# Optimization experiments

Hardware: AMD Instinct MI355X
Metric: run time of the kernel (lower is better)

## Reference

```python
import jax, jax.numpy as jnp
import numpy as np

RES = 32
EPS = 0.0


def setup_inputs() -> dict:
    key = jax.random.key(0)
    k1, k2 = jax.random.split(key)
    B, C, N = 32, 64, 8192
    features = jax.random.normal(k1, (B, C, N), dtype=jnp.float32)
    coords = jax.random.normal(k2, (B, 3, N), dtype=jnp.float32)
    return {"features": features, "coords": coords}


def reference(features, coords):
    R = RES
    B, C, N = features.shape
    # center coords per batch (mean over points)
    norm_coords = coords - jnp.mean(coords, axis=2, keepdims=True)  # [B,3,N]
    # normalize=True branch: divide by 2*max point L2 norm
    max_norm = jnp.max(jnp.linalg.norm(norm_coords, axis=1, keepdims=True),
                       axis=2, keepdims=True)  # [B,1,1]
    norm_coords = norm_coords / (max_norm * 2.0 + EPS) + 0.5
    # scale to voxel grid and clip
    norm_coords = jnp.clip(norm_coords * R, 0.0, R - 1)  # [B,3,N]
    vox = jnp.round(norm_coords).astype(jnp.int32)  # [B,3,N]
    # flat voxel index per point, offset per batch -> global segment id
    flat = (vox[:, 0] * R + vox[:, 1]) * R + vox[:, 2]  # [B,N]
    idx = (flat + jnp.arange(B, dtype=jnp.int32)[:, None] * (R ** 3)).reshape(-1)  # [B*N]
    num_seg = B * R ** 3
    cnt = jax.ops.segment_sum(jnp.ones((B * N,), features.dtype), idx,
                              num_segments=num_seg)  # [B*R^3]
    feat_pn = features.transpose(0, 2, 1).reshape(B * N, C)  # [B*N,C]
    sums = jax.ops.segment_sum(feat_pn, idx, num_segments=num_seg)  # [B*R^3,C]
    avg = sums / jnp.maximum(cnt, 1.0)[:, None]
    voxelized = avg.reshape(B, R, R, R, C).transpose(0, 4, 1, 2, 3)  # [B,C,R,R,R]
    return voxelized, norm_coords
```

## Files before the change

kernel.cpp:

```cpp
#include <hip/hip_runtime.h>

constexpr int B = 32, C = 64, N = 8192, R = 32, R3 = R * R * R;
constexpr int HALF = R3 / 2;
constexpr int T = 1024;
constexpr int PPT = N / T;

typedef float f32x4 __attribute__((ext_vector_type(4)));
typedef unsigned int u32x4 __attribute__((ext_vector_type(4)));

constexpr size_t IDX_OFF = 0;
constexpr size_t PF_OFF  = (size_t)B * N * 2;

__device__ __forceinline__ void lds_barrier() {
  asm volatile("s_waitcnt lgkmcnt(0)" ::: "memory");
  __builtin_amdgcn_s_barrier();
  __builtin_amdgcn_sched_barrier(0);
}

__global__ __launch_bounds__(1024) void prep_kernel(
    const float* __restrict__ coords, float* __restrict__ ncout,
    unsigned short* __restrict__ idx, float* __restrict__ pf) {
  __shared__ __align__(16) unsigned char smem[R3 * 4];
  double* sm = (double*)smem;
  float* smf = (float*)smem;
  unsigned int* cnt = (unsigned int*)smem;

  const int b = blockIdx.x;
  const int t = threadIdx.x;
  const float* cb = coords + (size_t)b * 3 * N;

  double sx = 0.0, sy = 0.0, sz = 0.0;
  for (int n = t; n < N; n += T) {
    sx += (double)cb[n];
    sy += (double)cb[N + n];
    sz += (double)cb[2 * N + n];
  }
  float mean[3];
  double vals[3] = {sx, sy, sz};
  for (int d = 0; d < 3; ++d) {
    sm[t] = vals[d];
    __syncthreads();
    for (int s = 512; s > 0; s >>= 1) {
      if (t < s) sm[t] += sm[t + s];
      __syncthreads();
    }
    mean[d] = (float)(sm[0] / (double)N);
    __syncthreads();
  }

  float mx = 0.0f;
  for (int n = t; n < N; n += T) {
    float dx = __fsub_rn(cb[n], mean[0]);
    float dy = __fsub_rn(cb[N + n], mean[1]);
    float dz = __fsub_rn(cb[2 * N + n], mean[2]);
    float n2 = __fadd_rn(__fadd_rn(__fmul_rn(dx, dx), __fmul_rn(dy, dy)),
                         __fmul_rn(dz, dz));
    mx = fmaxf(mx, n2);
  }
  smf[t] = mx;
  __syncthreads();
  for (int s = 512; s > 0; s >>= 1) {
    if (t < s) smf[t] = fmaxf(smf[t], smf[t + s]);
    __syncthreads();
  }
  const float dn = __fmul_rn(__fsqrt_rn(smf[0]), 2.0f);
  __syncthreads();

  const int n0 = t * PPT;
  const f32x4 xa = *(const f32x4*)(cb + n0);
  const f32x4 xc = *(const f32x4*)(cb + n0 + 4);
  const f32x4 ya = *(const f32x4*)(cb + N + n0);
  const f32x4 yc = *(const f32x4*)(cb + N + n0 + 4);
  const f32x4 za = *(const f32x4*)(cb + 2 * N + n0);
  const f32x4 zc = *(const f32x4*)(cb + 2 * N + n0 + 4);

  {
    u32x4* cz = (u32x4*)cnt;
    const u32x4 z4 = {0u, 0u, 0u, 0u};
#pragma unroll
    for (int k = 0; k < R3 / 4; k += T) cz[k + t] = z4;
  }
  lds_barrier();

  int iv[PPT];
  f32x4 o0[2], o1[2], o2[2];
#pragma unroll
  for (int h = 0; h < 2; ++h) {
    const f32x4 xs = h ? xc : xa;
    const f32x4 ys = h ? yc : ya;
    const f32x4 zs = h ? zc : za;
#pragma unroll
    for (int j = 0; j < 4; ++j) {
      float t0 = __fmul_rn(__fadd_rn(__fdiv_rn(__fsub_rn(xs[j], mean[0]), dn), 0.5f), 32.0f);
      float t1 = __fmul_rn(__fadd_rn(__fdiv_rn(__fsub_rn(ys[j], mean[1]), dn), 0.5f), 32.0f);
      float t2 = __fmul_rn(__fadd_rn(__fdiv_rn(__fsub_rn(zs[j], mean[2]), dn), 0.5f), 32.0f);
      t0 = fminf(fmaxf(t0, 0.0f), 31.0f);
      t1 = fminf(fmaxf(t1, 0.0f), 31.0f);
      t2 = fminf(fmaxf(t2, 0.0f), 31.0f);
      o0[h][j] = t0;
      o1[h][j] = t1;
      o2[h][j] = t2;
      const int vx = (int)rintf(t0);
      const int vy = (int)rintf(t1);
      const int vz = (int)rintf(t2);
      iv[h * 4 + j] = (vx * R + vy) * R + vz;
    }
  }

  float* nc = ncout + (size_t)b * 3 * N;
  __builtin_nontemporal_store(o0[0], (f32x4*)(nc + n0));
  __builtin_nontemporal_store(o0[1], (f32x4*)(nc + n0 + 4));
  __builtin_nontemporal_store(o1[0], (f32x4*)(nc + N + n0));
  __builtin_nontemporal_store(o1[1], (f32x4*)(nc + N + n0 + 4));
  __builtin_nontemporal_store(o2[0], (f32x4*)(nc + 2 * N + n0));
  __builtin_nontemporal_store(o2[1], (f32x4*)(nc + 2 * N + n0 + 4));

  {
    u32x4 iw = {(unsigned)iv[0] | ((unsigned)iv[1] << 16),
                (unsigned)iv[2] | ((unsigned)iv[3] << 16),
                (unsigned)iv[4] | ((unsigned)iv[5] << 16),
                (unsigned)iv[6] | ((unsigned)iv[7] << 16)};
    *(u32x4*)(idx + (size_t)b * N + n0) = iw;
  }

#pragma unroll
  for (int k = 0; k < PPT; ++k) atomicAdd(&cnt[iv[k]], 1u);
  lds_barrier();

  f32x4 q0, q1;
#pragma unroll
  for (int j = 0; j < 4; ++j) {
    q0[j] = __fdiv_rn(1.0f, (float)cnt[iv[j]]);
    q1[j] = __fdiv_rn(1.0f, (float)cnt[iv[4 + j]]);
  }
  *(f32x4*)(pf + (size_t)b * N + n0) = q0;
  *(f32x4*)(pf + (size_t)b * N + n0 + 4) = q1;
}

__global__ __launch_bounds__(1024, 8) void accum_kernel(
    const float* __restrict__ feats, const unsigned short* __restrict__ idx,
    const float* __restrict__ pf, float* __restrict__ voxout) {
  __shared__ float lds[HALF];
  const int blk = blockIdx.x;
  const int c = blk & (C - 1);
  const int b = blk >> 6;
  const int t = threadIdx.x;
  const int n0 = t * PPT;

  const unsigned short* ib = idx + (size_t)b * N;
  const float* pb = pf + (size_t)b * N;
  const float* fb = feats + ((size_t)b * C + c) * N;

  const u32x4 ip = *(const u32x4*)(ib + n0);
  const f32x4 p0 = *(const f32x4*)(pb + n0);
  const f32x4 p1 = *(const f32x4*)(pb + n0 + 4);
  const f32x4 f0 = __builtin_nontemporal_load((const f32x4*)(fb + n0));
  const f32x4 f1 = __builtin_nontemporal_load((const f32x4*)(fb + n0) + 1);

  int iv[PPT];
  float fv[PPT];
#pragma unroll
  for (int j = 0; j < 4; ++j) {
    iv[2 * j] = (int)(ip[j] & 0xffffu);
    iv[2 * j + 1] = (int)(ip[j] >> 16);
  }
#pragma unroll
  for (int j = 0; j < 4; ++j) {
    fv[j] = f0[j] * p0[j];
    fv[4 + j] = f1[j] * p1[j];
  }

  f32x4* lp = (f32x4*)lds;
  const f32x4 z = {0.f, 0.f, 0.f, 0.f};

  for (int h = 0; h < 2; ++h) {
    const int lo = h * HALF;

#pragma unroll
    for (int k = t; k < HALF / 4; k += T) lp[k] = z;
    lds_barrier();

#pragma unroll
    for (int k = 0; k < PPT; ++k) {
      const int loc = iv[k] - lo;
      if ((unsigned)loc < (unsigned)HALF) atomicAdd(&lds[loc], fv[k]);
    }
    lds_barrier();

    f32x4* ob4 = (f32x4*)(voxout + ((size_t)b * C + c) * R3 + lo);
#pragma unroll
    for (int v = t; v < HALF / 4; v += T)
      __builtin_nontemporal_store(lp[v], ob4 + v);
    if (h == 0) lds_barrier();
  }
}

extern "C" void kernel_launch(void* const* d_in, const int* in_sizes, int n_in,
                              void* d_out, int out_size, void* d_ws,
                              size_t ws_size, hipStream_t stream) {
  const float* feats  = (const float*)d_in[0];
  const float* coords = (const float*)d_in[1];

  float* voxout = (float*)d_out;
  float* ncout  = voxout + (size_t)B * C * R3;

  char* ws = (char*)d_ws;
  unsigned short* idx = (unsigned short*)(ws + IDX_OFF);
  float* pf           = (float*)(ws + PF_OFF);

  prep_kernel<<<B, 1024, 0, stream>>>(coords, ncout, idx, pf);
  accum_kernel<<<B * C, 1024, 0, stream>>>(feats, idx, pf, voxout);
}
```

Measured before the change: 366.7 us.

## Double-buffer LDS voxel accumulation in quarter slabs to overlap dump and scatter

The voxel grid per (batch, channel) block is now processed in four quarter-size slabs rather than two halves, alternating between two LDS buffers. Writing one slab out to global memory can then overlap with zeroing and scattering into the other buffer, which removes the trailing barrier between phases. Total LDS use is unchanged, so occupancy stays the same. In exchange, every point's index is range-checked four times instead of twice, and the kernel runs more barrier-separated phases overall.

```diff
diff --git a/kernel.cpp b/kernel.cpp
--- a/kernel.cpp
+++ b/kernel.cpp
@@ -1,7 +1,7 @@
 #include <hip/hip_runtime.h>
 
 constexpr int B = 32, C = 64, N = 8192, R = 32, R3 = R * R * R;
-constexpr int HALF = R3 / 2;
+constexpr int QUART = R3 / 4;
 constexpr int T = 1024;
 constexpr int PPT = N / T;
 
@@ -140,7 +140,7 @@
 __global__ __launch_bounds__(1024, 8) void accum_kernel(
     const float* __restrict__ feats, const unsigned short* __restrict__ idx,
     const float* __restrict__ pf, float* __restrict__ voxout) {
-  __shared__ float lds[HALF];
+  __shared__ float lds[2][QUART];
   const int blk = blockIdx.x;
   const int c = blk & (C - 1);
   const int b = blk >> 6;
@@ -170,29 +170,61 @@
     fv[4 + j] = f1[j] * p1[j];
   }
 
-  f32x4* lp = (f32x4*)lds;
+  f32x4* lp0 = (f32x4*)lds[0];
+  f32x4* lp1 = (f32x4*)lds[1];
   const f32x4 z = {0.f, 0.f, 0.f, 0.f};
-
-  for (int h = 0; h < 2; ++h) {
-    const int lo = h * HALF;
-
-#pragma unroll
-    for (int k = t; k < HALF / 4; k += T) lp[k] = z;
-    lds_barrier();
-
-#pragma unroll
-    for (int k = 0; k < PPT; ++k) {
-      const int loc = iv[k] - lo;
-      if ((unsigned)loc < (unsigned)HALF) atomicAdd(&lds[loc], fv[k]);
-    }
-    lds_barrier();
-
-    f32x4* ob4 = (f32x4*)(voxout + ((size_t)b * C + c) * R3 + lo);
-#pragma unroll
-    for (int v = t; v < HALF / 4; v += T)
-      __builtin_nontemporal_store(lp[v], ob4 + v);
-    if (h == 0) lds_barrier();
-  }
+  float* outb = voxout + ((size_t)b * C + c) * R3;
+
+#define ZERO_SLAB(LP)            \
+  do {                           \
+    (LP)[t] = z;                 \
+    (LP)[t + T] = z;             \
+  } while (0)
+
+#define SCATTER(BUF, LO)                                          \
+  do {                                                            \
+    _Pragma("unroll") for (int k = 0; k < PPT; ++k) {             \
+      const int loc = iv[k] - (LO);                               \
+      if ((unsigned)loc < (unsigned)QUART)                        \
+        atomicAdd(&(BUF)[loc], fv[k]);                            \
+    }                                                             \
+  } while (0)
+
+#define DUMP(LP, Q)                                               \
+  do {                                                            \
+    f32x4* ob4 = (f32x4*)(outb + (Q) * QUART);                    \
+    __builtin_nontemporal_store((LP)[t], ob4 + t);                \
+    __builtin_nontemporal_store((LP)[t + T], ob4 + t + T);        \
+  } while (0)
+
+  ZERO_SLAB(lp0);
+  lds_barrier();
+  SCATTER(lds[0], 0 * QUART);
+  lds_barrier();
+
+  DUMP(lp0, 0);
+  ZERO_SLAB(lp1);
+  lds_barrier();
+  SCATTER(lds[1], 1 * QUART);
+  lds_barrier();
+
+  DUMP(lp1, 1);
+  ZERO_SLAB(lp0);
+  lds_barrier();
+  SCATTER(lds[0], 2 * QUART);
+  lds_barrier();
+
+  DUMP(lp0, 2);
+  ZERO_SLAB(lp1);
+  lds_barrier();
+  SCATTER(lds[1], 3 * QUART);
+  lds_barrier();
+
+  DUMP(lp1, 3);
+
+#undef ZERO_SLAB
+#undef SCATTER
+#undef DUMP
 }
 
 extern "C" void kernel_launch(void* const* d_in, const int* in_sizes, int n_in,
```

New measurement: 366.7 us. No clear change (+0.0%).

## Shrink accum blocks to 512 threads with quarter-grid LDS passes; merge prep reductions

Applied to the files above, without the earlier changes.

The accumulation kernel now runs 512 threads per block, each handling 16 points, and scatters into a quarter-size LDS buffer (32 KB) over four passes instead of two halves of 64 KB. The smaller LDS footprint is meant to let more blocks reside per CU, so zeroing, atomics and streaming stores overlap across blocks. The cost is extra passes and barriers, and each pass re-tests every point against its range. The prep kernel also merges the three mean reductions into one combined tree and moves the count-histogram zeroing earlier so fewer barriers are needed.

```diff
diff --git a/kernel.cpp b/kernel.cpp
--- a/kernel.cpp
+++ b/kernel.cpp
@@ -1,9 +1,11 @@
 #include <hip/hip_runtime.h>
 
 constexpr int B = 32, C = 64, N = 8192, R = 32, R3 = R * R * R;
-constexpr int HALF = R3 / 2;
-constexpr int T = 1024;
-constexpr int PPT = N / T;
+constexpr int QUART = R3 / 4;
+constexpr int TP = 1024;
+constexpr int TA = 512;
+constexpr int PPTP = N / TP;
+constexpr int PPTA = N / TA;
 
 typedef float f32x4 __attribute__((ext_vector_type(4)));
 typedef unsigned int u32x4 __attribute__((ext_vector_type(4)));
@@ -20,36 +22,45 @@
 __global__ __launch_bounds__(1024) void prep_kernel(
     const float* __restrict__ coords, float* __restrict__ ncout,
     unsigned short* __restrict__ idx, float* __restrict__ pf) {
-  __shared__ __align__(16) unsigned char smem[R3 * 4];
-  double* sm = (double*)smem;
-  float* smf = (float*)smem;
-  unsigned int* cnt = (unsigned int*)smem;
+  __shared__ unsigned int cnt[R3];
+  __shared__ double sm3[3][TP];
+  __shared__ float smf[TP];
 
   const int b = blockIdx.x;
   const int t = threadIdx.x;
   const float* cb = coords + (size_t)b * 3 * N;
 
+  {
+    u32x4* cz = (u32x4*)cnt;
+    const u32x4 z4 = {0u, 0u, 0u, 0u};
+#pragma unroll
+    for (int k = 0; k < R3 / 4; k += TP) cz[k + t] = z4;
+  }
+
   double sx = 0.0, sy = 0.0, sz = 0.0;
-  for (int n = t; n < N; n += T) {
+  for (int n = t; n < N; n += TP) {
     sx += (double)cb[n];
     sy += (double)cb[N + n];
     sz += (double)cb[2 * N + n];
   }
+  sm3[0][t] = sx;
+  sm3[1][t] = sy;
+  sm3[2][t] = sz;
+  __syncthreads();
+  for (int s = 512; s > 0; s >>= 1) {
+    if (t < s) {
+      sm3[0][t] += sm3[0][t + s];
+      sm3[1][t] += sm3[1][t + s];
+      sm3[2][t] += sm3[2][t + s];
+    }
+    __syncthreads();
+  }
   float mean[3];
-  double vals[3] = {sx, sy, sz};
-  for (int d = 0; d < 3; ++d) {
-    sm[t] = vals[d];
-    __syncthreads();
-    for (int s = 512; s > 0; s >>= 1) {
-      if (t < s) sm[t] += sm[t + s];
-      __syncthreads();
-    }
-    mean[d] = (float)(sm[0] / (double)N);
-    __syncthreads();
-  }
+#pragma unroll
+  for (int d = 0; d < 3; ++d) mean[d] = (float)(sm3[d][0] / (double)N);
 
   float mx = 0.0f;
-  for (int n = t; n < N; n += T) {
+  for (int n = t; n < N; n += TP) {
     float dx = __fsub_rn(cb[n], mean[0]);
     float dy = __fsub_rn(cb[N + n], mean[1]);
     float dz = __fsub_rn(cb[2 * N + n], mean[2]);
@@ -64,9 +75,8 @@
     __syncthreads();
   }
   const float dn = __fmul_rn(__fsqrt_rn(smf[0]), 2.0f);
-  __syncthreads();
-
-  const int n0 = t * PPT;
+
+  const int n0 = t * PPTP;
   const f32x4 xa = *(const f32x4*)(cb + n0);
   const f32x4 xc = *(const f32x4*)(cb + n0 + 4);
   const f32x4 ya = *(const f32x4*)(cb + N + n0);
@@ -74,15 +84,7 @@
   const f32x4 za = *(const f32x4*)(cb + 2 * N + n0);
   const f32x4 zc = *(const f32x4*)(cb + 2 * N + n0 + 4);
 
-  {
-    u32x4* cz = (u32x4*)cnt;
-    const u32x4 z4 = {0u, 0u, 0u, 0u};
-#pragma unroll
-    for (int k = 0; k < R3 / 4; k += T) cz[k + t] = z4;
-  }
-  lds_barrier();
-
-  int iv[PPT];
+  int iv[PPTP];
   f32x4 o0[2], o1[2], o2[2];
 #pragma unroll
   for (int h = 0; h < 2; ++h) {
@@ -124,7 +126,7 @@
   }
 
 #pragma unroll
-  for (int k = 0; k < PPT; ++k) atomicAdd(&cnt[iv[k]], 1u);
+  for (int k = 0; k < PPTP; ++k) atomicAdd(&cnt[iv[k]], 1u);
   lds_barrier();
 
   f32x4 q0, q1;
@@ -137,61 +139,74 @@
   *(f32x4*)(pf + (size_t)b * N + n0 + 4) = q1;
 }
 
-__global__ __launch_bounds__(1024, 8) void accum_kernel(
+__global__ __launch_bounds__(512, 8) void accum_kernel(
     const float* __restrict__ feats, const unsigned short* __restrict__ idx,
     const float* __restrict__ pf, float* __restrict__ voxout) {
-  __shared__ float lds[HALF];
+  __shared__ float lds[QUART];
   const int blk = blockIdx.x;
   const int c = blk & (C - 1);
   const int b = blk >> 6;
   const int t = threadIdx.x;
-  const int n0 = t * PPT;
+  const int n0 = t * PPTA;
 
   const unsigned short* ib = idx + (size_t)b * N;
   const float* pb = pf + (size_t)b * N;
   const float* fb = feats + ((size_t)b * C + c) * N;
 
-  const u32x4 ip = *(const u32x4*)(ib + n0);
-  const f32x4 p0 = *(const f32x4*)(pb + n0);
-  const f32x4 p1 = *(const f32x4*)(pb + n0 + 4);
-  const f32x4 f0 = __builtin_nontemporal_load((const f32x4*)(fb + n0));
-  const f32x4 f1 = __builtin_nontemporal_load((const f32x4*)(fb + n0) + 1);
-
-  int iv[PPT];
-  float fv[PPT];
-#pragma unroll
-  for (int j = 0; j < 4; ++j) {
-    iv[2 * j] = (int)(ip[j] & 0xffffu);
-    iv[2 * j + 1] = (int)(ip[j] >> 16);
-  }
-#pragma unroll
-  for (int j = 0; j < 4; ++j) {
-    fv[j] = f0[j] * p0[j];
-    fv[4 + j] = f1[j] * p1[j];
+  int iv[PPTA];
+  float fv[PPTA];
+  {
+    const u32x4 ip = *(const u32x4*)(ib + n0);
+    const f32x4 p0 = *(const f32x4*)(pb + n0);
+    const f32x4 p1 = *(const f32x4*)(pb + n0 + 4);
+    const f32x4 f0 = __builtin_nontemporal_load((const f32x4*)(fb + n0));
+    const f32x4 f1 = __builtin_nontemporal_load((const f32x4*)(fb + n0) + 1);
+#pragma unroll
+    for (int j = 0; j < 4; ++j) {
+      iv[2 * j] = (int)(ip[j] & 0xffffu);
+      iv[2 * j + 1] = (int)(ip[j] >> 16);
+      fv[j] = f0[j] * p0[j];
+      fv[4 + j] = f1[j] * p1[j];
+    }
+  }
+  {
+    const u32x4 ip = *(const u32x4*)(ib + n0 + 8);
+    const f32x4 p0 = *(const f32x4*)(pb + n0 + 8);
+    const f32x4 p1 = *(const f32x4*)(pb + n0 + 12);
+    const f32x4 f0 = __builtin_nontemporal_load((const f32x4*)(fb + n0) + 2);
+    const f32x4 f1 = __builtin_nontemporal_load((const f32x4*)(fb + n0) + 3);
+#pragma unroll
+    for (int j = 0; j < 4; ++j) {
+      iv[8 + 2 * j] = (int)(ip[j] & 0xffffu);
+      iv[8 + 2 * j + 1] = (int)(ip[j] >> 16);
+      fv[8 + j] = f0[j] * p0[j];
+      fv[12 + j] = f1[j] * p1[j];
+    }
   }
 
   f32x4* lp = (f32x4*)lds;
   const f32x4 z = {0.f, 0.f, 0.f, 0.f};
-
-  for (int h = 0; h < 2; ++h) {
-    const int lo = h * HALF;
-
-#pragma unroll
-    for (int k = t; k < HALF / 4; k += T) lp[k] = z;
+  float* outb = voxout + ((size_t)b * C + c) * R3;
+
+  for (int q = 0; q < 4; ++q) {
+    const int lo = q * QUART;
+
+#pragma unroll
+    for (int k = 0; k < 4; ++k) lp[t + k * TA] = z;
     lds_barrier();
 
 #pragma unroll
-    for (int k = 0; k < PPT; ++k) {
+    for (int k = 0; k < PPTA; ++k) {
       const int loc = iv[k] - lo;
-      if ((unsigned)loc < (unsigned)HALF) atomicAdd(&lds[loc], fv[k]);
+      if ((unsigned)loc < (unsigned)QUART) atomicAdd(&lds[loc], fv[k]);
     }
     lds_barrier();
 
-    f32x4* ob4 = (f32x4*)(voxout + ((size_t)b * C + c) * R3 + lo);
-#pragma unroll
-    for (int v = t; v < HALF / 4; v += T)
-      __builtin_nontemporal_store(lp[v], ob4 + v);
-    if (h == 0) lds_barrier();
+    f32x4* ob4 = (f32x4*)(outb + lo);
+#pragma unroll
+    for (int k = 0; k < 4; ++k)
+      __builtin_nontemporal_store(lp[t + k * TA], ob4 + t + k * TA);
+    if (q < 3) lds_barrier();
   }
 }
 
@@ -208,6 +223,6 @@
   unsigned short* idx = (unsigned short*)(ws + IDX_OFF);
   float* pf           = (float*)(ws + PF_OFF);
 
-  prep_kernel<<<B, 1024, 0, stream>>>(coords, ncout, idx, pf);
-  accum_kernel<<<B * C, 1024, 0, stream>>>(feats, idx, pf, voxout);
-}
+  prep_kernel<<<B, TP, 0, stream>>>(coords, ncout, idx, pf);
+  accum_kernel<<<B * C, TA, 0, stream>>>(feats, idx, pf, voxout);
+}
```

Result: no change. 366.8 us (median of 2 runs) (+0.0%).
